# Performance work log

Hardware: AMD Instinct MI355X
Metric: run time of the kernel (lower is better)

The kernel has to match this reference:

```python
import jax, jax.numpy as jnp
import numpy as np

B, N, C, H = 4, 2048, 1024, 16
D = C // H

def setup_inputs() -> dict:
    key = jax.random.key(0)
    k1, k2, k3 = jax.random.split(key, 3)
    x = jax.random.normal(k1, (B, N, C), dtype=jnp.float32)
    w_qkv = jax.random.normal(k2, (C, 3 * C), dtype=jnp.float32) * (C ** -0.5)
    w_proj = jax.random.normal(k3, (C, C), dtype=jnp.float32) * (C ** -0.5)
    b_proj = jnp.zeros((C,), dtype=jnp.float32)
    return {"x": x, "w_qkv": w_qkv, "w_proj": w_proj, "b_proj": b_proj}

def reference(x, w_qkv, w_proj, b_proj):
    scale = D ** -0.5
    qkv = x @ w_qkv                                   # [B,N,3C]
    qkv = qkv.reshape(B, N, 3, H, D).transpose(2, 0, 3, 1, 4)  # [3,B,H,N,D]
    q, k, v = qkv[0], qkv[1], qkv[2]
    attn = jnp.einsum('bhnd,bhmd->bhnm', q, k) * scale  # [B,H,N,N]
    attn = jax.nn.softmax(attn, axis=-1)
    o = jnp.einsum('bhnm,bhmd->bhnd', attn, v)          # [B,H,N,D]
    o = o.transpose(0, 2, 1, 3).reshape(B, N, C)
    return o @ w_proj + b_proj
```

## Files before the change

### kernel.cpp

```cpp
#include <hip/hip_runtime.h>
#include <hip/hip_bf16.h>


#define B_ 4
#define N_ 2048
#define C_ 1024
#define H_ 16
#define D_ 64
#define MCONST 24.0f
#define QSCALE (0.125f * 1.44269504088896340736f)

typedef __attribute__((ext_vector_type(8))) __bf16 bf16x8;
typedef __attribute__((ext_vector_type(4))) float f32x4;
typedef __attribute__((ext_vector_type(16))) float f32x16;
typedef unsigned int u32;
typedef __attribute__((ext_vector_type(2))) u32 u32x2;
typedef __attribute__((ext_vector_type(4))) u32 u32x4;

__device__ inline unsigned short f2bf(float f) {
  __bf16 h = (__bf16)f;
  return __builtin_bit_cast(unsigned short, h);
}

__device__ __forceinline__ u32 pk2(float lo, float hi) {
  return (u32)f2bf(lo) | ((u32)f2bf(hi) << 16);
}

__device__ __forceinline__ void gld16(const void* g, void* l) {
  __builtin_amdgcn_global_load_lds(
      (const __attribute__((address_space(1))) u32*)g,
      (__attribute__((address_space(3))) u32*)l, 16, 0, 0);
}

__global__ __launch_bounds__(256) void cvt_bf16_kernel(
    const float* __restrict__ in, unsigned short* __restrict__ out) {
  int i = (blockIdx.x * 256 + threadIdx.x) * 8;
  float4 f0 = *(const float4*)&in[i];
  float4 f1 = *(const float4*)&in[i + 4];
  ushort4 h0, h1;
  h0.x = f2bf(f0.x); h0.y = f2bf(f0.y); h0.z = f2bf(f0.z); h0.w = f2bf(f0.w);
  h1.x = f2bf(f1.x); h1.y = f2bf(f1.y); h1.z = f2bf(f1.z); h1.w = f2bf(f1.w);
  *(ushort4*)&out[i] = h0;
  *(ushort4*)&out[i + 4] = h1;
}

__global__ __launch_bounds__(256) void transpose_cvt_kernel(
    const float* __restrict__ in, unsigned short* __restrict__ out,
    int K, int Nn) {
  __shared__ float tile[32][33];
  const int t = threadIdx.x;
  const int k0 = blockIdx.y * 32, n0 = blockIdx.x * 32;
  {
    int r = t >> 3, c = (t & 7) * 4;
    float4 f = *(const float4*)&in[(size_t)(k0 + r) * Nn + n0 + c];
    tile[r][c + 0] = f.x; tile[r][c + 1] = f.y;
    tile[r][c + 2] = f.z; tile[r][c + 3] = f.w;
  }
  __syncthreads();
  {
    int nr = t >> 3, kc = (t & 7) * 4;
    ushort4 h;
    h.x = f2bf(tile[kc + 0][nr]);
    h.y = f2bf(tile[kc + 1][nr]);
    h.z = f2bf(tile[kc + 2][nr]);
    h.w = f2bf(tile[kc + 3][nr]);
    *(ushort4*)&out[(size_t)(n0 + nr) * K + k0 + kc] = h;
  }
}

__global__ __launch_bounds__(512, 1) void gemm256_kernel(
    const unsigned short* __restrict__ A, const unsigned short* __restrict__ Bt,
    unsigned short* __restrict__ qb, unsigned short* __restrict__ kb,
    unsigned short* __restrict__ vtb, int M, int K, int Nout)
{
  __shared__ unsigned short LDS[3][2][256 * 32];
  const int tid = threadIdx.x;
  const int w = tid >> 6, lane = tid & 63;
  const int l15 = lane & 15, lk = lane >> 4;
  const int wm = w >> 2, wn = w & 3;
  const int wg = (blockIdx.x & 7) * 48 + (blockIdx.x >> 3);
  const int n0 = (wg % 12) * 256, m0 = (wg / 12) * 256;

  const int s_row = tid >> 2;
  const int s_col = ((tid & 3) * 8) ^ (((s_row >> 3) & 1) * 16);
  const int s_dst = tid * 8;
  const int kcol = (lk * 8) ^ (((l15 >> 3) & 1) * 16);

  f32x4 acc[8][4];
#pragma unroll
  for (int m = 0; m < 8; m++)
#pragma unroll
    for (int n = 0; n < 4; n++) acc[m][n] = f32x4{0.f, 0.f, 0.f, 0.f};

#pragma unroll
  for (int i = 0; i < 2; i++)
    gld16(&A[(size_t)(m0 + i * 128 + s_row) * K + s_col],
          &LDS[0][0][i * 4096 + s_dst]);
#pragma unroll
  for (int i = 0; i < 2; i++)
    gld16(&Bt[(size_t)(n0 + i * 128 + s_row) * K + s_col],
          &LDS[0][1][i * 4096 + s_dst]);

  int cur = 0;
  for (int j = 0; j < 31; ++j) {
    const int nxt = (cur + 1 == 3) ? 0 : cur + 1;
    const int kt = (j + 1) * 32;
#pragma unroll
    for (int i = 0; i < 2; i++)
      gld16(&A[(size_t)(m0 + i * 128 + s_row) * K + kt + s_col],
            &LDS[nxt][0][i * 4096 + s_dst]);
    asm volatile("s_waitcnt vmcnt(2)" ::: "memory");
    __builtin_amdgcn_s_barrier();
    asm volatile("" ::: "memory");

    bf16x8 bf[4], af[4];
#pragma unroll
    for (int n = 0; n < 4; n++)
      bf[n] = *(const bf16x8*)&LDS[cur][1][(wn * 64 + n * 16 + l15) * 32 + kcol];
#pragma unroll
    for (int m = 0; m < 4; m++)
      af[m] = *(const bf16x8*)&LDS[cur][0][(wm * 128 + m * 16 + l15) * 32 + kcol];
    __builtin_amdgcn_s_setprio(1);
#pragma unroll
    for (int m = 0; m < 4; m++)
#pragma unroll
      for (int n = 0; n < 4; n++)
        acc[m][n] = __builtin_amdgcn_mfma_f32_16x16x32_bf16(af[m], bf[n], acc[m][n], 0, 0, 0);
    __builtin_amdgcn_s_setprio(0);

#pragma unroll
    for (int i = 0; i < 2; i++)
      gld16(&Bt[(size_t)(n0 + i * 128 + s_row) * K + kt + s_col],
            &LDS[nxt][1][i * 4096 + s_dst]);

#pragma unroll
    for (int m = 0; m < 4; m++)
      af[m] = *(const bf16x8*)&LDS[cur][0][(wm * 128 + (m + 4) * 16 + l15) * 32 + kcol];
    __builtin_amdgcn_s_setprio(1);
#pragma unroll
    for (int m = 0; m < 4; m++)
#pragma unroll
      for (int n = 0; n < 4; n++)
        acc[m + 4][n] = __builtin_amdgcn_mfma_f32_16x16x32_bf16(af[m], bf[n], acc[m + 4][n], 0, 0, 0);
    __builtin_amdgcn_s_setprio(0);
    cur = nxt;
  }

  asm volatile("s_waitcnt vmcnt(0)" ::: "memory");
  __builtin_amdgcn_s_barrier();
  asm volatile("" ::: "memory");
  {
    bf16x8 bf[4], af[4];
#pragma unroll
    for (int n = 0; n < 4; n++)
      bf[n] = *(const bf16x8*)&LDS[cur][1][(wn * 64 + n * 16 + l15) * 32 + kcol];
#pragma unroll
    for (int m = 0; m < 4; m++)
      af[m] = *(const bf16x8*)&LDS[cur][0][(wm * 128 + m * 16 + l15) * 32 + kcol];
#pragma unroll
    for (int m = 0; m < 4; m++)
#pragma unroll
      for (int n = 0; n < 4; n++)
        acc[m][n] = __builtin_amdgcn_mfma_f32_16x16x32_bf16(af[m], bf[n], acc[m][n], 0, 0, 0);
#pragma unroll
    for (int m = 0; m < 4; m++)
      af[m] = *(const bf16x8*)&LDS[cur][0][(wm * 128 + (m + 4) * 16 + l15) * 32 + kcol];
#pragma unroll
    for (int m = 0; m < 4; m++)
#pragma unroll
      for (int n = 0; n < 4; n++)
        acc[m + 4][n] = __builtin_amdgcn_mfma_f32_16x16x32_bf16(af[m], bf[n], acc[m + 4][n], 0, 0, 0);
  }

#pragma unroll
  for (int n = 0; n < 4; n++) {
    int c = n0 + wn * 64 + n * 16 + l15;
    int tsel = c >> 10, h = (c >> 6) & 15, d = c & 63;
    if (tsel < 2) {
      unsigned short* dst = (tsel == 0) ? qb : kb;
      float sc = (tsel == 0) ? QSCALE : 1.0f;
#pragma unroll
      for (int m = 0; m < 8; m++) {
#pragma unroll
        for (int r = 0; r < 4; r++) {
          int row = m0 + wm * 128 + m * 16 + lk * 4 + r;
          int b = row >> 11, nn = row & 2047;
          dst[(((size_t)(b * 16 + h)) * 2048 + nn) * 64 + d] = f2bf(acc[m][n][r] * sc);
        }
      }
    } else {
#pragma unroll
      for (int m = 0; m < 8; m++) {
        int row0 = m0 + wm * 128 + m * 16 + lk * 4;
        int b = row0 >> 11, nn = row0 & 2047;
        ushort4 pv;
        pv.x = f2bf(acc[m][n][0]); pv.y = f2bf(acc[m][n][1]);
        pv.z = f2bf(acc[m][n][2]); pv.w = f2bf(acc[m][n][3]);
        *(ushort4*)&vtb[(((size_t)(b * 16 + h)) * 64 + d) * 2048 + nn] = pv;
      }
    }
  }
}

__global__ __launch_bounds__(512, 1) void gemmproj_kernel(
    const unsigned short* __restrict__ A, const unsigned short* __restrict__ Bt,
    const float* __restrict__ bias, float* __restrict__ outp,
    int M, int K, int Nout)
{
  __shared__ unsigned short LDS[3][12288];
  const int tid = threadIdx.x;
  const int w = tid >> 6, lane = tid & 63;
  const int l15 = lane & 15, lk = lane >> 4;
  const int wm = w >> 1, wn = w & 1;
  const int n0 = blockIdx.x * 128, m0 = blockIdx.y * 256;

  const int s_row = tid >> 2;
  const int s_col = ((tid & 3) * 8) ^ (((s_row >> 3) & 1) * 16);
  const int s_dst = tid * 8;
  const int kcol = (lk * 8) ^ (((l15 >> 3) & 1) * 16);

  f32x4 acc[4][4];
#pragma unroll
  for (int m = 0; m < 4; m++)
#pragma unroll
    for (int n = 0; n < 4; n++) acc[m][n] = f32x4{0.f, 0.f, 0.f, 0.f};

#pragma unroll
  for (int i = 0; i < 2; i++)
    gld16(&A[(size_t)(m0 + i * 128 + s_row) * K + s_col],
          &LDS[0][i * 4096 + s_dst]);
  gld16(&Bt[(size_t)(n0 + s_row) * K + s_col], &LDS[0][8192 + s_dst]);

  int cur = 0;
  for (int j = 0; j < 31; ++j) {
    const int nxt = (cur + 1 == 3) ? 0 : cur + 1;
    const int kt = (j + 1) * 32;
#pragma unroll
    for (int i = 0; i < 2; i++)
      gld16(&A[(size_t)(m0 + i * 128 + s_row) * K + kt + s_col],
            &LDS[nxt][i * 4096 + s_dst]);
    asm volatile("s_waitcnt vmcnt(2)" ::: "memory");
    __builtin_amdgcn_s_barrier();
    asm volatile("" ::: "memory");

    bf16x8 bf[4], af[2];
#pragma unroll
    for (int n = 0; n < 4; n++)
      bf[n] = *(const bf16x8*)&LDS[cur][8192 + (wn * 64 + n * 16 + l15) * 32 + kcol];
#pragma unroll
    for (int m = 0; m < 2; m++)
      af[m] = *(const bf16x8*)&LDS[cur][(wm * 64 + m * 16 + l15) * 32 + kcol];
    __builtin_amdgcn_s_setprio(1);
#pragma unroll
    for (int m = 0; m < 2; m++)
#pragma unroll
      for (int n = 0; n < 4; n++)
        acc[m][n] = __builtin_amdgcn_mfma_f32_16x16x32_bf16(af[m], bf[n], acc[m][n], 0, 0, 0);
    __builtin_amdgcn_s_setprio(0);

    gld16(&Bt[(size_t)(n0 + s_row) * K + kt + s_col], &LDS[nxt][8192 + s_dst]);

#pragma unroll
    for (int m = 0; m < 2; m++)
      af[m] = *(const bf16x8*)&LDS[cur][(wm * 64 + (m + 2) * 16 + l15) * 32 + kcol];
    __builtin_amdgcn_s_setprio(1);
#pragma unroll
    for (int m = 0; m < 2; m++)
#pragma unroll
      for (int n = 0; n < 4; n++)
        acc[m + 2][n] = __builtin_amdgcn_mfma_f32_16x16x32_bf16(af[m], bf[n], acc[m + 2][n], 0, 0, 0);
    __builtin_amdgcn_s_setprio(0);
    cur = nxt;
  }

  asm volatile("s_waitcnt vmcnt(0)" ::: "memory");
  __builtin_amdgcn_s_barrier();
  asm volatile("" ::: "memory");
  {
    bf16x8 bf[4], af[2];
#pragma unroll
    for (int n = 0; n < 4; n++)
      bf[n] = *(const bf16x8*)&LDS[cur][8192 + (wn * 64 + n * 16 + l15) * 32 + kcol];
#pragma unroll
    for (int m = 0; m < 2; m++)
      af[m] = *(const bf16x8*)&LDS[cur][(wm * 64 + m * 16 + l15) * 32 + kcol];
#pragma unroll
    for (int m = 0; m < 2; m++)
#pragma unroll
      for (int n = 0; n < 4; n++)
        acc[m][n] = __builtin_amdgcn_mfma_f32_16x16x32_bf16(af[m], bf[n], acc[m][n], 0, 0, 0);
#pragma unroll
    for (int m = 0; m < 2; m++)
      af[m] = *(const bf16x8*)&LDS[cur][(wm * 64 + (m + 2) * 16 + l15) * 32 + kcol];
#pragma unroll
    for (int m = 0; m < 2; m++)
#pragma unroll
      for (int n = 0; n < 4; n++)
        acc[m + 2][n] = __builtin_amdgcn_mfma_f32_16x16x32_bf16(af[m], bf[n], acc[m + 2][n], 0, 0, 0);
  }

#pragma unroll
  for (int n = 0; n < 4; n++) {
    int c = n0 + wn * 64 + n * 16 + l15;
    float bv = bias[c];
#pragma unroll
    for (int m = 0; m < 4; m++) {
#pragma unroll
      for (int r = 0; r < 4; r++) {
        int row = m0 + wm * 64 + m * 16 + lk * 4 + r;
        outp[(size_t)row * Nout + c] = acc[m][n][r] + bv;
      }
    }
  }
}

__global__ __launch_bounds__(512) void flash_kernel(
    const unsigned short* __restrict__ qb, const unsigned short* __restrict__ kb,
    const unsigned short* __restrict__ vtb, unsigned short* __restrict__ ob)
{
  __shared__ unsigned short KVs[2][2][2][64 * 64];
  __shared__ float Lf[2][128];
  float* scratch = (float*)&KVs[0][0][0][0];

  const int tid = threadIdx.x;
  const int w = tid >> 6;
  const int lane = tid & 63;
  const int l31 = lane & 31;
  const int hi = lane >> 5;
  const int g = w >> 2;
  const int ws = w & 3;
  const int bh = blockIdx.x;
  const int q0 = blockIdx.y * 128;
  const size_t base = (size_t)bh * N_ * D_;
  const unsigned short* Qg = qb + base;
  const unsigned short* Kg = kb + base;
  const unsigned short* Vtg = vtb + base;

  const int t8 = tid & 255;
  const int s_r = t8 >> 3;
  const int s_sl = (t8 & 7) ^ (s_r & 7);
  const int swz = (lane & 7) << 3;

  const int qrow_g = q0 + ws * 32 + l31;
  bf16x8 qf[4];
#pragma unroll
  for (int ds = 0; ds < 4; ds++)
    qf[ds] = *(const bf16x8*)&Qg[(size_t)qrow_g * 64 + ds * 16 + hi * 8];

  f32x16 acc0, acc1, minit;
#pragma unroll
  for (int i = 0; i < 16; i++) { acc0[i] = 0.f; acc1[i] = 0.f; minit[i] = -MCONST; }
  float lrow = 0.f;

  const int kvbeg = g * (N_ / 2);

#pragma unroll
  for (int i = 0; i < 2; i++)
    gld16(&Kg[(size_t)(kvbeg + i * 32 + s_r) * 64 + s_sl * 8],
          &KVs[g][0][0][i * 2048 + ws * 512]);
#pragma unroll
  for (int i = 0; i < 2; i++)
    gld16(&Vtg[(size_t)(i * 32 + s_r) * N_ + kvbeg + s_sl * 8],
          &KVs[g][0][1][i * 2048 + ws * 512]);

  int cur = 0;
  for (int it = 0; it < 16; ++it) {
    __syncthreads();

    if (it + 1 < 16) {
      int kvn = kvbeg + (it + 1) * 64;
#pragma unroll
      for (int i = 0; i < 2; i++)
        gld16(&Kg[(size_t)(kvn + i * 32 + s_r) * 64 + s_sl * 8],
              &KVs[g][cur ^ 1][0][i * 2048 + ws * 512]);
#pragma unroll
      for (int i = 0; i < 2; i++)
        gld16(&Vtg[(size_t)(i * 32 + s_r) * N_ + kvn + s_sl * 8],
              &KVs[g][cur ^ 1][1][i * 2048 + ws * 512]);
    }

    const unsigned short* Kl = &KVs[g][cur][0][0];
    const unsigned short* Vl = &KVs[g][cur][1][0];

    u32 F[4][4];
#pragma unroll
    for (int t = 0; t < 2; t++) {
      f32x16 sa = minit;
      __builtin_amdgcn_s_setprio(1);
#pragma unroll
      for (int ds = 0; ds < 4; ds++) {
        bf16x8 a = *(const bf16x8*)&Kl[(t * 32 + l31) * 64 + ((ds * 16 + hi * 8) ^ swz)];
        sa = __builtin_amdgcn_mfma_f32_32x32x16_bf16(a, qf[ds], sa, 0, 0, 0);
      }
      __builtin_amdgcn_s_setprio(0);

      float p[16];
#pragma unroll
      for (int r = 0; r < 16; r++) p[r] = __builtin_amdgcn_exp2f(sa[r]);
      lrow += ((p[0] + p[1]) + (p[2] + p[3])) + ((p[4] + p[5]) + (p[6] + p[7]))
            + ((p[8] + p[9]) + (p[10] + p[11])) + ((p[12] + p[13]) + (p[14] + p[15]));

      u32 pk[8];
#pragma unroll
      for (int j = 0; j < 8; j++) pk[j] = pk2(p[2 * j], p[2 * j + 1]);
#if __has_builtin(__builtin_amdgcn_permlane32_swap)
      u32x2 r02 = __builtin_amdgcn_permlane32_swap(pk[0], pk[2], false, false);
      u32x2 r13 = __builtin_amdgcn_permlane32_swap(pk[1], pk[3], false, false);
      u32x2 r46 = __builtin_amdgcn_permlane32_swap(pk[4], pk[6], false, false);
      u32x2 r57 = __builtin_amdgcn_permlane32_swap(pk[5], pk[7], false, false);
      F[2 * t][0] = r02[0]; F[2 * t][2] = r02[1];
      F[2 * t][1] = r13[0]; F[2 * t][3] = r13[1];
      F[2 * t + 1][0] = r46[0]; F[2 * t + 1][2] = r46[1];
      F[2 * t + 1][1] = r57[0]; F[2 * t + 1][3] = r57[1];
#else
      u32 sw[8];
#pragma unroll
      for (int j = 0; j < 8; j++) sw[j] = (u32)__shfl_xor((int)pk[j], 32);
      F[2 * t][0] = hi ? sw[2] : pk[0];
      F[2 * t][1] = hi ? sw[3] : pk[1];
      F[2 * t][2] = hi ? pk[2] : sw[0];
      F[2 * t][3] = hi ? pk[3] : sw[1];
      F[2 * t + 1][0] = hi ? sw[6] : pk[4];
      F[2 * t + 1][1] = hi ? sw[7] : pk[5];
      F[2 * t + 1][2] = hi ? pk[6] : sw[4];
      F[2 * t + 1][3] = hi ? pk[7] : sw[5];
#endif
    }

    __builtin_amdgcn_s_setprio(1);
#pragma unroll
    for (int ks = 0; ks < 4; ks++) {
      u32x4 fv = {F[ks][0], F[ks][1], F[ks][2], F[ks][3]};
      bf16x8 a = __builtin_bit_cast(bf16x8, fv);
      bf16x8 b0 = *(const bf16x8*)&Vl[(0 * 32 + l31) * 64 + ((ks * 16 + hi * 8) ^ swz)];
      acc0 = __builtin_amdgcn_mfma_f32_32x32x16_bf16(a, b0, acc0, 0, 0, 0);
      bf16x8 b1 = *(const bf16x8*)&Vl[(1 * 32 + l31) * 64 + ((ks * 16 + hi * 8) ^ swz)];
      acc1 = __builtin_amdgcn_mfma_f32_32x32x16_bf16(a, b1, acc1, 0, 0, 0);
    }
    __builtin_amdgcn_s_setprio(0);
    cur ^= 1;
  }

  float rs = lrow + __shfl_xor(lrow, 32);
  if (lane < 32) Lf[g][ws * 32 + l31] = rs;
  __syncthreads();

  if (g == 0) {
#pragma unroll
    for (int r = 0; r < 16; r++) {
      int qr = (r & 3) + 8 * (r >> 2) + 4 * hi;
      scratch[(ws * 32 + qr) * 64 + l31]      = acc0[r];
      scratch[(ws * 32 + qr) * 64 + 32 + l31] = acc1[r];
    }
  }
  __syncthreads();
  if (g == 1) {
    const int b = bh >> 4, h = bh & 15;
#pragma unroll
    for (int r = 0; r < 16; r++) {
      int qr = (r & 3) + 8 * (r >> 2) + 4 * hi;
      float inv = 1.0f / (Lf[0][ws * 32 + qr] + Lf[1][ws * 32 + qr]);
      float o0 = scratch[(ws * 32 + qr) * 64 + l31]      + acc0[r];
      float o1 = scratch[(ws * 32 + qr) * 64 + 32 + l31] + acc1[r];
      int nq = q0 + ws * 32 + qr;
      size_t ob0 = (((size_t)b * N_ + nq) * H_ + h) * D_;
      ob[ob0 + l31]      = f2bf(o0 * inv);
      ob[ob0 + 32 + l31] = f2bf(o1 * inv);
    }
  }
}

extern "C" void kernel_launch(void* const* d_in, const int* in_sizes, int n_in,
                              void* d_out, int out_size, void* d_ws, size_t ws_size,
                              hipStream_t stream) {
  const float* x      = (const float*)d_in[0];
  const float* w_qkv  = (const float*)d_in[1];
  const float* w_proj = (const float*)d_in[2];
  const float* b_proj = (const float*)d_in[3];
  float* out = (float*)d_out;

  const size_t qsz = (size_t)B_ * H_ * N_ * D_;
  unsigned short* qb     = (unsigned short*)d_ws;
  unsigned short* kb     = qb + qsz;
  unsigned short* vtb    = kb + qsz;
  unsigned short* xbf    = vtb + qsz;
  unsigned short* ob     = xbf;
  unsigned short* wqkv_t = xbf + qsz;
  unsigned short* wproj_t= wqkv_t + (size_t)3072 * 1024;

  cvt_bf16_kernel<<<4096, 256, 0, stream>>>(x, xbf);
  transpose_cvt_kernel<<<dim3(3072 / 32, 1024 / 32), 256, 0, stream>>>(w_qkv, wqkv_t, 1024, 3072);
  transpose_cvt_kernel<<<dim3(1024 / 32, 1024 / 32), 256, 0, stream>>>(w_proj, wproj_t, 1024, 1024);

  gemm256_kernel<<<384, 512, 0, stream>>>(
      xbf, wqkv_t, qb, kb, vtb, 8192, 1024, 3072);

  flash_kernel<<<dim3(B_ * H_, N_ / 128), 512, 0, stream>>>(qb, kb, vtb, ob);

  gemmproj_kernel<<<dim3(1024 / 128, 8192 / 256), 512, 0, stream>>>(
      ob, wproj_t, b_proj, out, 8192, 1024, 1024);
}
```

Measured before the change: 211.6 us.

## Load K tiles directly from global into registers instead of LDS

K fragments are now read straight from global memory into registers, with the next tile prefetched after the QK/softmax phase. Only V stays staged in shared memory, which halves LDS use and removes the LDS reads for K. The cost is more register pressure and uncoalesced per-lane global loads of K. Each of the four waves in a group now issues redundant global loads for the same K rows, where the shared copy was loaded once per block.

New measurement: 293.4 us. 1.39x slower.

```diff
diff --git a/kernel.cpp b/kernel.cpp
--- a/kernel.cpp
+++ b/kernel.cpp
@@ -318,9 +318,9 @@
     const unsigned short* __restrict__ qb, const unsigned short* __restrict__ kb,
     const unsigned short* __restrict__ vtb, unsigned short* __restrict__ ob)
 {
-  __shared__ unsigned short KVs[2][2][2][64 * 64];
+  __shared__ unsigned short Vs[2][2][64 * 64];
   __shared__ float Lf[2][128];
-  float* scratch = (float*)&KVs[0][0][0][0];
+  float* scratch = (float*)&Vs[0][0][0];
 
   const int tid = threadIdx.x;
   const int w = tid >> 6;
@@ -356,12 +356,14 @@
 
 #pragma unroll
   for (int i = 0; i < 2; i++)
-    gld16(&Kg[(size_t)(kvbeg + i * 32 + s_r) * 64 + s_sl * 8],
-          &KVs[g][0][0][i * 2048 + ws * 512]);
-#pragma unroll
-  for (int i = 0; i < 2; i++)
     gld16(&Vtg[(size_t)(i * 32 + s_r) * N_ + kvbeg + s_sl * 8],
-          &KVs[g][0][1][i * 2048 + ws * 512]);
+          &Vs[g][0][i * 2048 + ws * 512]);
+  bf16x8 kreg[2][4];
+#pragma unroll
+  for (int t = 0; t < 2; t++)
+#pragma unroll
+    for (int ds = 0; ds < 4; ds++)
+      kreg[t][ds] = *(const bf16x8*)&Kg[(size_t)(kvbeg + t * 32 + l31) * 64 + ds * 16 + hi * 8];
 
   int cur = 0;
   for (int it = 0; it < 16; ++it) {
@@ -371,16 +373,11 @@
       int kvn = kvbeg + (it + 1) * 64;
 #pragma unroll
       for (int i = 0; i < 2; i++)
-        gld16(&Kg[(size_t)(kvn + i * 32 + s_r) * 64 + s_sl * 8],
-              &KVs[g][cur ^ 1][0][i * 2048 + ws * 512]);
-#pragma unroll
-      for (int i = 0; i < 2; i++)
         gld16(&Vtg[(size_t)(i * 32 + s_r) * N_ + kvn + s_sl * 8],
-              &KVs[g][cur ^ 1][1][i * 2048 + ws * 512]);
-    }
-
-    const unsigned short* Kl = &KVs[g][cur][0][0];
-    const unsigned short* Vl = &KVs[g][cur][1][0];
+              &Vs[g][cur ^ 1][i * 2048 + ws * 512]);
+    }
+
+    const unsigned short* Vl = &Vs[g][cur][0];
 
     u32 F[4][4];
 #pragma unroll
@@ -388,10 +385,8 @@
       f32x16 sa = minit;
       __builtin_amdgcn_s_setprio(1);
 #pragma unroll
-      for (int ds = 0; ds < 4; ds++) {
-        bf16x8 a = *(const bf16x8*)&Kl[(t * 32 + l31) * 64 + ((ds * 16 + hi * 8) ^ swz)];
-        sa = __builtin_amdgcn_mfma_f32_32x32x16_bf16(a, qf[ds], sa, 0, 0, 0);
-      }
+      for (int ds = 0; ds < 4; ds++)
+        sa = __builtin_amdgcn_mfma_f32_32x32x16_bf16(kreg[t][ds], qf[ds], sa, 0, 0, 0);
       __builtin_amdgcn_s_setprio(0);
 
       float p[16];
@@ -427,6 +422,15 @@
 #endif
     }
 
+    if (it + 1 < 16) {
+      int kvn = kvbeg + (it + 1) * 64;
+#pragma unroll
+      for (int t = 0; t < 2; t++)
+#pragma unroll
+        for (int ds = 0; ds < 4; ds++)
+          kreg[t][ds] = *(const bf16x8*)&Kg[(size_t)(kvn + t * 32 + l31) * 64 + ds * 16 + hi * 8];
+    }
+
     __builtin_amdgcn_s_setprio(1);
 #pragma unroll
     for (int ks = 0; ks < 4; ks++) {
```
